# Kernel optimization log

Measured on AMD Instinct MI355X. Metric: run time of the kernel, lower is better.

The kernel has to match this reference:

```python
import jax, jax.numpy as jnp
import numpy as np
from jax import lax


def _ramp_filter_real(size):
    # torch ramp_filter: spatial-domain ramp, FFT is purely real (even symmetric)
    image_n = np.concatenate([np.arange(1, size // 2 + 1, 2),
                              np.arange(size // 2 - 1, 0, -2)]).astype(np.float64)
    f = np.zeros(size, dtype=np.float64)
    f[0] = 0.25
    f[1::2] = -1.0 / (np.pi * image_n) ** 2
    return (2.0 * np.real(np.fft.fft(f))).astype(np.float32)  # [size]


def setup_inputs() -> dict:
    key = jax.random.key(0)
    # sinogram: [B, C, detector_bins, n_angles]
    x = jax.random.normal(key, (4, 1, 512, 180), dtype=jnp.float32)
    return {"x": x}


def reference(x):
    B, C, S, A = x.shape  # S = in_size = it_size (circle=True), A = n_angles
    # ---- ramp filtering along detector axis (axis=2) ----
    pad_to = max(64, 1 << int(np.ceil(np.log2(2 * S))))
    xp = jnp.pad(x, ((0, 0), (0, 0), (0, pad_to - S), (0, 0)))
    ramp = jnp.asarray(_ramp_filter_real(pad_to))
    # original multiplies by complex filter r*(1+i); imag part of ifft is 0 for real x,
    # so real part equals standard ramp filtering
    Xf = jnp.fft.fft(xp, axis=2)
    filt = (ramp * (1.0 + 1.0j)).astype(jnp.complex64)
    xfilt = jnp.real(jnp.fft.ifft(Xf * filt[None, None, :, None], axis=2))
    xfilt = xfilt[:, :, :S, :].astype(x.dtype)  # [B,C,S,A]

    # ---- backprojection ----
    unit = jnp.linspace(-1.0, 1.0, S, dtype=x.dtype)
    ygrid, xgrid = jnp.meshgrid(unit, unit, indexing="ij")  # torch.meshgrid 'ij'
    thetas = (jnp.arange(A, dtype=x.dtype) * (np.pi / 180.0)).astype(x.dtype)
    # t coordinate in [-sqrt2, sqrt2]: [A,S,S]
    t = (xgrid[None] * jnp.cos(thetas)[:, None, None]
         - ygrid[None] * jnp.sin(thetas)[:, None, None])
    # grid_sample bilinear, align_corners=True, zeros padding; X coord selects angle i exactly
    p = (t + 1.0) * 0.5 * (S - 1)
    p0 = jnp.floor(p)
    w = (p - p0).astype(x.dtype)
    i0 = p0.astype(jnp.int32)
    i1 = i0 + 1
    v0 = ((i0 >= 0) & (i0 < S)).astype(x.dtype)
    v1 = ((i1 >= 0) & (i1 < S)).astype(x.dtype)
    i0c = jnp.clip(i0, 0, S - 1)
    i1c = jnp.clip(i1, 0, S - 1)

    xa = jnp.moveaxis(xfilt, 3, 0)  # [A,B,C,S]

    def body(acc, inp):
        xa_a, i0a, i1a, wa, v0a, v1a = inp
        g = (xa_a[:, :, i0a] * v0a * (1.0 - wa)
             + xa_a[:, :, i1a] * v1a * wa)  # [B,C,S,S]
        return acc + g, None

    reco0 = jnp.zeros((B, C, S, S), dtype=x.dtype)
    reco, _ = lax.scan(body, reco0, (xa, i0c, i1c, w, v0, v1))

    # circle mask + normalization
    mask = (xgrid ** 2 + ygrid ** 2) <= 1.0
    reco = jnp.where(mask[None, None], reco, 0.0)
    reco = reco * (np.pi / (2.0 * A))
    return reco
```

## Files before the change

### kernel.cpp

```cpp
#include <hip/hip_runtime.h>
#include <hip/hip_fp16.h>
#include <math.h>

namespace {

constexpr int BB  = 4;
constexpr int SS  = 512;
constexpr int AA  = 180;
constexpr int PAD = 112;

typedef float v2f __attribute__((ext_vector_type(2)));

__global__ __launch_bounds__(256) void ramp_zero_kernel(
    const float* __restrict__ x, __half2* __restrict__ xf2, float* __restrict__ out) {
  const int t = threadIdx.x;
  {
    const int bid = blockIdx.y * 90 + blockIdx.x;
    float4 z = make_float4(0.f, 0.f, 0.f, 0.f);
    for (int i = bid * 256 + t; i < (BB * SS * SS) / 4; i += 360 * 256)
      ((float4*)out)[i] = z;
  }

  __shared__ __align__(16) float xs[2][2][256];
  __shared__ __align__(16) float G[2][528];
  __shared__ float yb[2][512];
  const int a0 = blockIdx.x * 2;
  const int b  = blockIdx.y;

  const float s  = (float)(M_PI / 360.0);
  const float cc = (float)(-2.0 / (M_PI * M_PI)) * s;
  for (int i = t; i < 528; i += 256) {
    { int kk = i;     float d = (float)(2 * kk - 511); G[0][i] = (kk < 512) ? cc / (d * d) : 0.0f; }
    { int kk = i + 1; float d = (float)(2 * kk - 511); G[1][i] = (kk < 512) ? cc / (d * d) : 0.0f; }
  }

  const float* xb = x + (size_t)b * (SS * AA) + a0;
  {
    int m = t;
    float2 v = *(const float2*)(xb + (size_t)m * AA);
    xs[0][m & 1][m >> 1] = v.x;  xs[1][m & 1][m >> 1] = v.y;
    m = t + 256;
    float2 v2 = *(const float2*)(xb + (size_t)m * AA);
    xs[0][m & 1][m >> 1] = v2.x; xs[1][m & 1][m >> 1] = v2.y;
  }
  __syncthreads();

  const int col = t >> 7;
  const int p   = (t >> 6) & 1;
  const int idx = t & 63;
  const float* Gp = G[p];
  const float* xv = xs[col][1 - p];

  float acc[4] = {0.f, 0.f, 0.f, 0.f};
  float W[8];
  {
    const int A0 = 4 * idx + 252;
    float4 w0 = *(const float4*)(Gp + A0);
    float4 w1 = *(const float4*)(Gp + A0 + 4);
    W[0] = w0.x; W[1] = w0.y; W[2] = w0.z; W[3] = w0.w;
    W[4] = w1.x; W[5] = w1.y; W[6] = w1.z; W[7] = w1.w;
  }

#pragma unroll
  for (int q = 0; q < 64; ++q) {
    const float4 xq = *(const float4*)(xv + 4 * q);
    float4 nw;
    if (q != 63) nw = *(const float4*)(Gp + (4 * idx + 252 - 4 * (q + 1)));
#pragma unroll
    for (int r = 0; r < 4; ++r) {
      acc[r] = fmaf(W[3 + r], xq.x, acc[r]);
      acc[r] = fmaf(W[2 + r], xq.y, acc[r]);
      acc[r] = fmaf(W[1 + r], xq.z, acc[r]);
      acc[r] = fmaf(W[0 + r], xq.w, acc[r]);
    }
    if (q != 63) {
      W[7] = W[3]; W[6] = W[2]; W[5] = W[1]; W[4] = W[0];
      W[0] = nw.x; W[1] = nw.y; W[2] = nw.z; W[3] = nw.w;
    }
  }

  const float selfc = 0.5f * s;
  const float* xsp = xs[col][p];
#pragma unroll
  for (int r = 0; r < 4; ++r)
    yb[col][p + 8 * idx + 2 * r] = fmaf(selfc, xsp[4 * idx + r], acc[r]);
  __syncthreads();

  __half2* orow = xf2 + ((size_t)(b * AA + a0)) * SS;
#pragma unroll
  for (int e = 0; e < 2; ++e) {
    int j = t + e * 256;
#pragma unroll
    for (int c2 = 0; c2 < 2; ++c2)
      orow[c2 * SS + j] = __floats2half2_rn(yb[c2][j], yb[c2][511 - j]);
  }
}

__global__ __launch_bounds__(256, 8) void backproject_kernel(
    const __half2* __restrict__ xf2, float* __restrict__ out) {
  __shared__ __align__(16) __half2 P2[2][3][768];
  __shared__ float2 trig[45];

  const int t     = threadIdx.x;
  const int w     = t >> 6;
  const int lane  = t & 63;
  const int tx    = blockIdx.x;
  const int ty    = blockIdx.y;
  const int b     = blockIdx.z >> 2;
  const int chunk = blockIdx.z & 3;
  const int a0    = chunk * 45;

  {
    const float step = 2.0f / 511.0f;
    float x0 = -1.0f + (float)(tx * 64) * step, x1 = -1.0f + (float)(tx * 64 + 63) * step;
    float y0 = -1.0f + (float)(ty * 16) * step, y1 = -1.0f + (float)(ty * 16 + 15) * step;
    float mx = (x0 <= 0.f && x1 >= 0.f) ? 0.f : fminf(fabsf(x0), fabsf(x1));
    float my = (y0 <= 0.f && y1 >= 0.f) ? 0.f : fminf(fabsf(y0), fabsf(y1));
    if (mx * mx + my * my > 1.0f) return;
  }

  {
    const __half2 hz = __floats2half2_rn(0.f, 0.f);
    for (int i = t; i < 6 * 256; i += 256) {
      int slot = i >> 8;
      int o    = i & 255;
      int j    = (o < PAD) ? o : (o + SS);
      P2[slot / 3][slot % 3][j] = hz;
    }
  }
  if (t < 45) {
    float th = (float)(a0 + t) * (float)(M_PI / 180.0);
    float sn, cn;
    sincosf(th, &sn, &cn);
    trig[t] = make_float2(cn * 255.5f, sn * 255.5f);
  }

  const __half2* src = xf2 + ((size_t)b * AA + a0) * SS;

  auto stage = [&](int g, int buf) {
    const __half2* base = src + (size_t)(g * 3) * SS;
    {
      const int sg = w;
      const __half2* gp = base + (sg >> 1) * SS + (sg & 1) * 256 + lane * 4;
      void* lp = (void*)&P2[buf][sg >> 1][PAD + (sg & 1) * 256];
      __builtin_amdgcn_global_load_lds(
          (const __attribute__((address_space(1))) void*)gp,
          (__attribute__((address_space(3))) void*)lp, 16, 0, 0);
    }
    if (w < 2) {
      const int sg = 4 + w;
      const __half2* gp = base + (sg >> 1) * SS + (sg & 1) * 256 + lane * 4;
      void* lp = (void*)&P2[buf][sg >> 1][PAD + (sg & 1) * 256];
      __builtin_amdgcn_global_load_lds(
          (const __attribute__((address_space(1))) void*)gp,
          (__attribute__((address_space(3))) void*)lp, 16, 0, 0);
    }
  };

  const int gx = tx * 64 + lane;
  const float step = 2.0f / 511.0f;
  const float xg = __fadd_rn(-1.0f, __fmul_rn((float)gx, step));
  float dy[4];
#pragma unroll
  for (int kk = 0; kk < 4; ++kk) {
    int gy = ty * 16 + w + 4 * kk;
    dy[kk] = -__fadd_rn(-1.0f, __fmul_rn((float)gy, step));
  }

  const float Kp = 255.5f + (float)PAD;
  v2f acc[4];
#pragma unroll
  for (int kk = 0; kk < 4; ++kk) acc[kk] = (v2f){0.f, 0.f};

  stage(0, 0);
  __syncthreads();

  const __half2 hz2 = __floats2half2_rn(0.f, 0.f);
  int buf = 0;
  for (int g = 0; g < 15; ++g) {
    if (g + 1 < 15) stage(g + 1, buf ^ 1);
    __half2 gacc[4] = {hz2, hz2, hz2, hz2};
#pragma unroll
    for (int aa = 0; aa < 3; ++aa) {
      const float2 cs = trig[g * 3 + aa];
      const float base = fmaf(xg, cs.x, Kp);
      const __half2* R = P2[buf][aa];
#pragma unroll
      for (int kk = 0; kk < 4; ++kk) {
        float p = fmaf(dy[kk], cs.y, base);
        int   I = (int)p;
#if __has_builtin(__builtin_amdgcn_fractf)
        float wq = __builtin_amdgcn_fractf(p);
#else
        float wq = p - floorf(p);
#endif
        struct { __half2 a, b; } q;
        __builtin_memcpy(&q, R + I, 8);
        __half2 dv  = __hsub2(q.b, q.a);
        __half2 wh2 = __floats2half2_rn(wq, wq);
        gacc[kk] = __hadd2(gacc[kk], __hfma2(wh2, dv, q.a));
      }
    }
#pragma unroll
    for (int kk = 0; kk < 4; ++kk) {
      float2 f = __half22float2(gacc[kk]);
      acc[kk].x += f.x;
      acc[kk].y += f.y;
    }
    __syncthreads();
    buf ^= 1;
  }

  const int gxm  = 511 - gx;
  const float xgm = __fadd_rn(-1.0f, __fmul_rn((float)gxm, step));
  const float xx  = __fmul_rn(xg, xg);
  const float xxm = __fmul_rn(xgm, xgm);
#pragma unroll
  for (int kk = 0; kk < 4; ++kk) {
    int gy  = ty * 16 + w + 4 * kk;
    float yg = -dy[kk];
    float s0 = __fadd_rn(xx, __fmul_rn(yg, yg));
    if (s0 <= 1.0f)
      unsafeAtomicAdd(&out[((size_t)b * SS + gy) * SS + gx], acc[kk].x);
    int gym = 511 - gy;
    float ygm = __fadd_rn(-1.0f, __fmul_rn((float)gym, step));
    float s1 = __fadd_rn(xxm, __fmul_rn(ygm, ygm));
    if (s1 <= 1.0f)
      unsafeAtomicAdd(&out[((size_t)b * SS + gym) * SS + gxm], acc[kk].y);
  }
}

}

extern "C" void kernel_launch(void* const* d_in, const int* in_sizes, int n_in,
                              void* d_out, int out_size, void* d_ws, size_t ws_size,
                              hipStream_t stream) {
  const float* x   = (const float*)d_in[0];
  float*       out = (float*)d_out;
  __half2*     xf2 = (__half2*)d_ws;

  ramp_zero_kernel<<<dim3(AA / 2, BB), 256, 0, stream>>>(x, xf2, out);
  backproject_kernel<<<dim3(4, 32, 16), 256, 0, stream>>>(xf2, out);
}
```

Before: 93.32 us.

## Gather backprojection samples directly from padded global rows instead of LDS staging

The filtered sinogram rows are written with a small zero-padded stride so the backprojection kernel can gather samples straight from global memory (through cache), with clamped indices. This drops the LDS double-buffer, async global-to-LDS copies and per-group barriers, and regroups angles five at a time. The cost is that each gather becomes a cached global load instead of an LDS read, which may raise latency. The clamp adds a little ALU work.

```diff
diff --git a/kernel.cpp b/kernel.cpp
--- a/kernel.cpp
+++ b/kernel.cpp
@@ -7,7 +7,7 @@
 constexpr int BB  = 4;
 constexpr int SS  = 512;
 constexpr int AA  = 180;
-constexpr int PAD = 112;
+constexpr int RST = 520;
 
 typedef float v2f __attribute__((ext_vector_type(2)));
 
@@ -86,19 +86,23 @@
     yb[col][p + 8 * idx + 2 * r] = fmaf(selfc, xsp[4 * idx + r], acc[r]);
   __syncthreads();
 
-  __half2* orow = xf2 + ((size_t)(b * AA + a0)) * SS;
+  __half2* orow = xf2 + (size_t)(b * AA + a0) * RST;
 #pragma unroll
   for (int e = 0; e < 2; ++e) {
     int j = t + e * 256;
 #pragma unroll
     for (int c2 = 0; c2 < 2; ++c2)
-      orow[c2 * SS + j] = __floats2half2_rn(yb[c2][j], yb[c2][511 - j]);
+      orow[c2 * RST + 4 + j] = __floats2half2_rn(yb[c2][j], yb[c2][511 - j]);
+  }
+  if (t < 16) {
+    int c2 = t >> 3, o = t & 7;
+    int j = (o < 4) ? o : (512 + o);
+    orow[c2 * RST + j] = __floats2half2_rn(0.f, 0.f);
   }
 }
 
 __global__ __launch_bounds__(256, 8) void backproject_kernel(
     const __half2* __restrict__ xf2, float* __restrict__ out) {
-  __shared__ __align__(16) __half2 P2[2][3][768];
   __shared__ float2 trig[45];
 
   const int t     = threadIdx.x;
@@ -119,43 +123,15 @@
     if (mx * mx + my * my > 1.0f) return;
   }
 
-  {
-    const __half2 hz = __floats2half2_rn(0.f, 0.f);
-    for (int i = t; i < 6 * 256; i += 256) {
-      int slot = i >> 8;
-      int o    = i & 255;
-      int j    = (o < PAD) ? o : (o + SS);
-      P2[slot / 3][slot % 3][j] = hz;
-    }
-  }
   if (t < 45) {
     float th = (float)(a0 + t) * (float)(M_PI / 180.0);
     float sn, cn;
     sincosf(th, &sn, &cn);
     trig[t] = make_float2(cn * 255.5f, sn * 255.5f);
   }
-
-  const __half2* src = xf2 + ((size_t)b * AA + a0) * SS;
-
-  auto stage = [&](int g, int buf) {
-    const __half2* base = src + (size_t)(g * 3) * SS;
-    {
-      const int sg = w;
-      const __half2* gp = base + (sg >> 1) * SS + (sg & 1) * 256 + lane * 4;
-      void* lp = (void*)&P2[buf][sg >> 1][PAD + (sg & 1) * 256];
-      __builtin_amdgcn_global_load_lds(
-          (const __attribute__((address_space(1))) void*)gp,
-          (__attribute__((address_space(3))) void*)lp, 16, 0, 0);
-    }
-    if (w < 2) {
-      const int sg = 4 + w;
-      const __half2* gp = base + (sg >> 1) * SS + (sg & 1) * 256 + lane * 4;
-      void* lp = (void*)&P2[buf][sg >> 1][PAD + (sg & 1) * 256];
-      __builtin_amdgcn_global_load_lds(
-          (const __attribute__((address_space(1))) void*)gp,
-          (__attribute__((address_space(3))) void*)lp, 16, 0, 0);
-    }
-  };
+  __syncthreads();
+
+  const __half2* src = xf2 + (size_t)(b * AA + a0) * RST;
 
   const int gx = tx * 64 + lane;
   const float step = 2.0f / 511.0f;
@@ -167,32 +143,29 @@
     dy[kk] = -__fadd_rn(-1.0f, __fmul_rn((float)gy, step));
   }
 
-  const float Kp = 255.5f + (float)PAD;
+  const float Kb = 255.5f + 4.0f;
   v2f acc[4];
 #pragma unroll
   for (int kk = 0; kk < 4; ++kk) acc[kk] = (v2f){0.f, 0.f};
 
-  stage(0, 0);
-  __syncthreads();
-
   const __half2 hz2 = __floats2half2_rn(0.f, 0.f);
-  int buf = 0;
-  for (int g = 0; g < 15; ++g) {
-    if (g + 1 < 15) stage(g + 1, buf ^ 1);
+  for (int g = 0; g < 9; ++g) {
     __half2 gacc[4] = {hz2, hz2, hz2, hz2};
 #pragma unroll
-    for (int aa = 0; aa < 3; ++aa) {
-      const float2 cs = trig[g * 3 + aa];
-      const float base = fmaf(xg, cs.x, Kp);
-      const __half2* R = P2[buf][aa];
+    for (int aa = 0; aa < 5; ++aa) {
+      const int a = g * 5 + aa;
+      const float2 cs = trig[a];
+      const float base = fmaf(xg, cs.x, Kb);
+      const __half2* R = src + a * RST;
 #pragma unroll
       for (int kk = 0; kk < 4; ++kk) {
-        float p = fmaf(dy[kk], cs.y, base);
-        int   I = (int)p;
+        float P = fmaf(dy[kk], cs.y, base);
+        int   I = (int)P;
+        I = min(max(I, 0), 518);
 #if __has_builtin(__builtin_amdgcn_fractf)
-        float wq = __builtin_amdgcn_fractf(p);
+        float wq = __builtin_amdgcn_fractf(P);
 #else
-        float wq = p - floorf(p);
+        float wq = P - floorf(P);
 #endif
         struct { __half2 a, b; } q;
         __builtin_memcpy(&q, R + I, 8);
@@ -207,8 +180,6 @@
       acc[kk].x += f.x;
       acc[kk].y += f.y;
     }
-    __syncthreads();
-    buf ^= 1;
   }
 
   const int gxm  = 511 - gx;
```

Result: slower. 119.5 us (+28.1%).
